# Optimization experiments

Measured on AMD Instinct MI355X. Metric: run time of the kernel, lower is better.

## Reference

```python
import jax, jax.numpy as jnp
import numpy as np

IN_F = 4096
OUT_F = 4096
WBITS = 4      # weight bits
ABITS = 4      # input (activation) bits; T=4 -> L=ceil(15/4)=4 spike levels/step
EPS = 1e-8


def fwht(x):
    """Normalized fast Walsh-Hadamard transform over the last dim (K=1 case of
    matmul_hadU_cuda): y = H_n @ x / sqrt(n), n a power of 2."""
    n = x.shape[-1]
    m = int(np.log2(n))
    shape = x.shape
    x = x.reshape((-1,) + (2,) * m)  # [B, 2,2,...,2]
    for ax in range(1, m + 1):       # fixed log2(n) butterfly stages
        a = jnp.take(x, 0, axis=ax)
        b = jnp.take(x, 1, axis=ax)
        x = jnp.stack([a + b, a - b], axis=ax)
    return x.reshape(shape) * np.float32(1.0 / np.sqrt(n))


def quant_weight(w):
    """Per-output-channel symmetric RTN fake-quant to WBITS, with STE."""
    qmax = 2 ** (WBITS - 1) - 1  # 7
    scale = jnp.maximum(jnp.max(jnp.abs(w), axis=1, keepdims=True) / qmax, EPS)
    q = jnp.clip(jnp.round(w / scale), -qmax - 1, qmax)
    wq = q * scale
    return w + jax.lax.stop_gradient(wq - w)


def quant_act(x):
    """LMHT spiking input quantizer: dynamic asymmetric fake-quant to ABITS.
    Over T steps the neuron emits up to L levels/step, summing to the integer
    code q in [0, 2^ABITS-1]; the (averaged) dequantized output equals
    (q - zp) * scale. STE for gradient."""
    levels = 2 ** ABITS - 1  # 15
    xmin = jnp.min(x)
    xmax = jnp.max(x)
    scale = jnp.maximum((xmax - xmin) / levels, EPS)
    zp = jnp.round(-xmin / scale)
    q = jnp.clip(jnp.round(x / scale) + zp, 0, levels)
    xq = (q - zp) * scale
    return x + jax.lax.stop_gradient(xq - x)


def setup_inputs() -> dict:
    key = jax.random.key(0)
    k1, k2, k3 = jax.random.split(key, 3)
    x = jax.random.normal(k1, (4, 2048, IN_F), dtype=jnp.float32)
    weight = jax.random.normal(k2, (OUT_F, IN_F), dtype=jnp.float32) * 0.02
    bias = jax.random.normal(k3, (OUT_F,), dtype=jnp.float32) * 0.01
    return {"x": x, "weight": weight, "bias": bias}


def reference(x, weight, bias):
    # online full Hadamard rotation of the input
    x = fwht(x)
    # weight fake-quant (W4) and activation fake-quant (A4, LMHT neuron)
    wq = quant_weight(weight)
    xq = quant_act(x)
    # F.linear: out = xq @ wq.T + bias
    out = jnp.einsum('bsi,oi->bso', xq, wq) + bias
    return out
```

## Files before the change

### kernel.cpp

```cpp
#include <hip/hip_runtime.h>
#include <stdint.h>
#include <stddef.h>


typedef __attribute__((ext_vector_type(4))) int int4v;
typedef __attribute__((ext_vector_type(4))) float float4v;

#define EPSQ 1e-8f

__device__ __forceinline__ void fwht_wave(float (&e)[64], int l) {
#pragma unroll
    for (int s = 32; s >= 4; s >>= 1)
#pragma unroll
        for (int j = 0; j < 64; ++j)
            if ((j & s) == 0) {
                float a = e[j], b = e[j + s];
                e[j] = a + b;
                e[j + s] = a - b;
            }
#pragma unroll
    for (int m = 32; m >= 1; m >>= 1) {
        float sgn = (l & m) ? -1.0f : 1.0f;
#pragma unroll
        for (int j = 0; j < 64; ++j) {
            float t = __shfl_xor(e[j], m);
            e[j] = fmaf(sgn, e[j], t);
        }
    }
#pragma unroll
    for (int s = 2; s >= 1; s >>= 1)
#pragma unroll
        for (int j = 0; j < 64; ++j)
            if ((j & s) == 0) {
                float a = e[j], b = e[j + s];
                e[j] = a + b;
                e[j + s] = a - b;
            }
}

__global__ __launch_bounds__(256) void k_fwht_store(
    const float* __restrict__ x, float* __restrict__ y,
    float2* __restrict__ wmm) {
    int l = threadIdx.x & 63, w = threadIdx.x >> 6;
    int row = blockIdx.x * 4 + w;
    const float4v* xv = (const float4v*)(x + (size_t)row * 4096);
    float e[64];
#pragma unroll
    for (int q = 0; q < 16; ++q) {
        float4v v = xv[q * 64 + l];
        e[4 * q + 0] = v[0]; e[4 * q + 1] = v[1];
        e[4 * q + 2] = v[2]; e[4 * q + 3] = v[3];
    }
    fwht_wave(e, l);
#pragma unroll
    for (int j = 0; j < 64; ++j) e[j] *= 0.015625f;

    float4v* yv = (float4v*)(y + (size_t)row * 4096);
#pragma unroll
    for (int q = 0; q < 16; ++q) {
        float4v v;
        v[0] = e[4 * q + 0]; v[1] = e[4 * q + 1];
        v[2] = e[4 * q + 2]; v[3] = e[4 * q + 3];
        yv[q * 64 + l] = v;
    }
    float mn = e[0], mx = e[0];
#pragma unroll
    for (int j = 1; j < 64; ++j) { mn = fminf(mn, e[j]); mx = fmaxf(mx, e[j]); }
#pragma unroll
    for (int m = 32; m >= 1; m >>= 1) {
        mn = fminf(mn, __shfl_xor(mn, m));
        mx = fmaxf(mx, __shfl_xor(mx, m));
    }
    if (l == 0) wmm[row] = make_float2(mn, mx);
}

__global__ __launch_bounds__(256) void k_mmred(const float2* __restrict__ wmm,
                                               float* __restrict__ mm) {
    __shared__ float red[8];
    int t = threadIdx.x;
    float mn = INFINITY, mx = -INFINITY;
    for (int i = t; i < 8192; i += 256) {
        float2 v = wmm[i];
        mn = fminf(mn, v.x);
        mx = fmaxf(mx, v.y);
    }
#pragma unroll
    for (int m = 32; m >= 1; m >>= 1) {
        mn = fminf(mn, __shfl_xor(mn, m));
        mx = fmaxf(mx, __shfl_xor(mx, m));
    }
    if ((t & 63) == 0) { red[(t >> 6) * 2] = mn; red[(t >> 6) * 2 + 1] = mx; }
    __syncthreads();
    if (t == 0) {
#pragma unroll
        for (int wv = 1; wv < 4; ++wv) {
            mn = fminf(mn, red[wv * 2]);
            mx = fmaxf(mx, red[wv * 2 + 1]);
        }
        mm[0] = mn;
        mm[1] = mx;
    }
}

__global__ __launch_bounds__(256) void k_quant_x(
    const float* __restrict__ y, const float* __restrict__ mm,
    int8_t* __restrict__ xq) {
    float xmin = mm[0], xmax = mm[1];
    float scale = fmaxf((xmax - xmin) / 15.0f, EPSQ);
    float zp = rintf(-xmin / scale);
    int izp = (int)zp;

    const float4v* yv = (const float4v*)y;
    int* q = (int*)xq;
    const size_t n4 = (size_t)8192 * 4096 / 4;
    const size_t stride = (size_t)2048 * 256;
    for (size_t i = (size_t)blockIdx.x * 256 + threadIdx.x; i < n4;
         i += stride) {
        float4v v = yv[i];
        int pk = 0;
#pragma unroll
        for (int r = 0; r < 4; ++r) {
            float qq = rintf(v[r] / scale) + zp;
            qq = fminf(fmaxf(qq, 0.0f), 15.0f);
            int code = (int)qq - izp;
            pk |= (code & 0xFF) << (8 * r);
        }
        q[i] = pk;
    }
}

__global__ __launch_bounds__(256) void k_quant_w(
    const float* __restrict__ wgt, int8_t* __restrict__ wq,
    float* __restrict__ sw) {
    __shared__ float red[4];
    int o = blockIdx.x, t = threadIdx.x;
    const float4v* wv = (const float4v*)(wgt + (size_t)o * 4096);
    float4v a0 = wv[t * 4 + 0], a1 = wv[t * 4 + 1],
            a2 = wv[t * 4 + 2], a3 = wv[t * 4 + 3];
    float am = 0.0f;
#pragma unroll
    for (int r = 0; r < 4; ++r)
        am = fmaxf(am, fmaxf(fmaxf(fabsf(a0[r]), fabsf(a1[r])),
                             fmaxf(fabsf(a2[r]), fabsf(a3[r]))));
#pragma unroll
    for (int m = 32; m >= 1; m >>= 1) am = fmaxf(am, __shfl_xor(am, m));
    if ((t & 63) == 0) red[t >> 6] = am;
    __syncthreads();
    am = fmaxf(fmaxf(red[0], red[1]), fmaxf(red[2], red[3]));

    float scale = fmaxf(am / 7.0f, EPSQ);
    if (t == 0) sw[o] = scale;

    int4v pk;
#pragma unroll
    for (int k = 0; k < 4; ++k) {
        float4v a = (k == 0) ? a0 : (k == 1) ? a1 : (k == 2) ? a2 : a3;
        int p = 0;
#pragma unroll
        for (int r = 0; r < 4; ++r) {
            float q = rintf(a[r] / scale);
            q = fminf(fmaxf(q, -8.0f), 7.0f);
            p |= ((int)q & 0xFF) << (8 * r);
        }
        pk[k] = p;
    }
    *(int4v*)(wq + (size_t)o * 4096 + t * 16) = pk;
}

#define BM 128
#define BN 128
#define BKq 64

__global__ __launch_bounds__(256) void k_gemm(
    const int8_t* __restrict__ A,
    const int8_t* __restrict__ B,
    const float* __restrict__ sw, const float* __restrict__ bias,
    const float* __restrict__ mm, float* __restrict__ C) {
    constexpr int N = 4096, K = 4096;
    __shared__ __align__(16) int8_t As[BM * BKq];
    __shared__ __align__(16) int8_t Bs[BN * BKq];

    int tid = threadIdx.x;
    int m0 = (blockIdx.x >> 5) * BM;
    int n0 = (blockIdx.x & 31) * BN;
    int w = tid >> 6, l = tid & 63;
    int wr = w >> 1, wc = w & 1;
    int kg = l >> 4, lr = l & 15;

    int4v acc[4][4] = {};

    for (int k0 = 0; k0 < K; k0 += BKq) {
#pragma unroll
        for (int it = 0; it < 2; ++it) {
            int idx = it * 256 + tid;
            int row = idx >> 2;
            int ccs = (idx & 3) ^ ((row >> 1) & 3);
            __builtin_amdgcn_global_load_lds(
                (const __attribute__((address_space(1))) void*)
                    (A + (size_t)(m0 + row) * K + k0 + ccs * 16),
                (__attribute__((address_space(3))) void*)(As + idx * 16),
                16, 0, 0);
            __builtin_amdgcn_global_load_lds(
                (const __attribute__((address_space(1))) void*)
                    (B + (size_t)(n0 + row) * K + k0 + ccs * 16),
                (__attribute__((address_space(3))) void*)(Bs + idx * 16),
                16, 0, 0);
        }
        __syncthreads();

        int4v af[4], bf[4];
#pragma unroll
        for (int i = 0; i < 4; ++i) {
            int ra = wr * 64 + i * 16 + lr;
            int rb = wc * 64 + i * 16 + lr;
            af[i] = *(const int4v*)(As + ra * BKq +
                                    ((kg ^ ((ra >> 1) & 3)) * 16));
            bf[i] = *(const int4v*)(Bs + rb * BKq +
                                    ((kg ^ ((rb >> 1) & 3)) * 16));
        }
#pragma unroll
        for (int i = 0; i < 4; ++i)
#pragma unroll
            for (int j = 0; j < 4; ++j)
                acc[i][j] = __builtin_amdgcn_mfma_i32_16x16x64_i8(
                    af[i], bf[j], acc[i][j], 0, 0, 0);
        __syncthreads();
    }

    float xmin = mm[0], xmax = mm[1];
    float sx = fmaxf((xmax - xmin) / 15.0f, EPSQ);

#pragma unroll
    for (int j = 0; j < 4; ++j) {
        int col = n0 + wc * 64 + j * 16 + lr;
        float s = sx * sw[col];
        float bz = bias[col];
#pragma unroll
        for (int i = 0; i < 4; ++i) {
            int rowb = m0 + wr * 64 + i * 16 + kg * 4;
#pragma unroll
            for (int r = 0; r < 4; ++r)
                C[(size_t)(rowb + r) * N + col] =
                    (float)acc[i][j][r] * s + bz;
        }
    }
}

extern "C" void kernel_launch(void* const* d_in, const int* in_sizes, int n_in,
                              void* d_out, int out_size, void* d_ws,
                              size_t ws_size, hipStream_t stream) {
    const float* x = (const float*)d_in[0];
    const float* weight = (const float*)d_in[1];
    const float* bias = (const float*)d_in[2];
    float* out = (float*)d_out;

    char* ws = (char*)d_ws;
    float* mm = (float*)ws;
    float2* wmm = (float2*)(ws + 1024);
    float* sw = (float*)(ws + 131072);
    int8_t* xq = (int8_t*)(ws + (1 << 20));
    int8_t* wq = (int8_t*)(ws + (1 << 20) + ((size_t)8192 * 4096));

    float* y = out;

    hipLaunchKernelGGL(k_fwht_store, dim3(2048), dim3(256), 0, stream,
                       x, y, wmm);
    hipLaunchKernelGGL(k_mmred, dim3(1), dim3(256), 0, stream, wmm, mm);
    hipLaunchKernelGGL(k_quant_w, dim3(4096), dim3(256), 0, stream,
                       weight, wq, sw);
    hipLaunchKernelGGL(k_quant_x, dim3(2048), dim3(256), 0, stream,
                       y, mm, xq);
    hipLaunchKernelGGL(k_gemm, dim3(64 * 32), dim3(256), 0, stream,
                       xq, wq, sw, bias, mm, out);
}
```

Measured before the change: 465.9 us.

## Replace cross-lane shuffle FWHT with LDS transpose and two in-register H64 passes

The Walsh-Hadamard transform previously used 6 rounds of 64 cross-lane shuffles per wave. It now does a 64-point butterfly in registers, transposes through a swizzled shared-memory tile, and does a second 64-point butterfly, treating H4096 as H64 ⊗ H64. This removes the shuffle traffic but adds 64 KB of LDS per block, which limits occupancy, and makes the input loads strided scalar reads. The min/max reduction now launches 1024 threads and the activation quantizer uses twice as many blocks.

```diff
diff --git a/kernel.cpp b/kernel.cpp
--- a/kernel.cpp
+++ b/kernel.cpp
@@ -8,9 +8,9 @@
 
 #define EPSQ 1e-8f
 
-__device__ __forceinline__ void fwht_wave(float (&e)[64], int l) {
-#pragma unroll
-    for (int s = 32; s >= 4; s >>= 1)
+__device__ __forceinline__ void h64(float (&e)[64]) {
+#pragma unroll
+    for (int s = 32; s >= 1; s >>= 1)
 #pragma unroll
         for (int j = 0; j < 64; ++j)
             if ((j & s) == 0) {
@@ -18,51 +18,52 @@
                 e[j] = a + b;
                 e[j + s] = a - b;
             }
-#pragma unroll
-    for (int m = 32; m >= 1; m >>= 1) {
-        float sgn = (l & m) ? -1.0f : 1.0f;
-#pragma unroll
-        for (int j = 0; j < 64; ++j) {
-            float t = __shfl_xor(e[j], m);
-            e[j] = fmaf(sgn, e[j], t);
-        }
-    }
-#pragma unroll
-    for (int s = 2; s >= 1; s >>= 1)
-#pragma unroll
-        for (int j = 0; j < 64; ++j)
-            if ((j & s) == 0) {
-                float a = e[j], b = e[j + s];
-                e[j] = a + b;
-                e[j + s] = a - b;
-            }
-}
-
-__global__ __launch_bounds__(256) void k_fwht_store(
+}
+
+__global__ __launch_bounds__(256) void k_fwht(
     const float* __restrict__ x, float* __restrict__ y,
     float2* __restrict__ wmm) {
+    __shared__ float tile[4][4096];
     int l = threadIdx.x & 63, w = threadIdx.x >> 6;
     int row = blockIdx.x * 4 + w;
-    const float4v* xv = (const float4v*)(x + (size_t)row * 4096);
+    const float* xr = x + (size_t)row * 4096;
+
     float e[64];
 #pragma unroll
-    for (int q = 0; q < 16; ++q) {
-        float4v v = xv[q * 64 + l];
-        e[4 * q + 0] = v[0]; e[4 * q + 1] = v[1];
-        e[4 * q + 2] = v[2]; e[4 * q + 3] = v[3];
-    }
-    fwht_wave(e, l);
+    for (int a = 0; a < 64; ++a) e[a] = xr[a * 64 + l];
+
+    h64(e);
+
+    float* T = tile[w];
+#pragma unroll
+    for (int t = 0; t < 16; ++t) {
+        float4v v;
+        v[0] = e[4 * t + 0]; v[1] = e[4 * t + 1];
+        v[2] = e[4 * t + 2]; v[3] = e[4 * t + 3];
+        *(float4v*)(T + l * 64 + 4 * ((t + l) & 15)) = v;
+    }
+    __syncthreads();
+    {
+        int t0 = l >> 2, j0 = l & 3;
+#pragma unroll
+        for (int b = 0; b < 64; ++b)
+            e[b] = T[b * 64 + 4 * ((t0 + b) & 15) + j0];
+    }
+
+    h64(e);
+
 #pragma unroll
     for (int j = 0; j < 64; ++j) e[j] *= 0.015625f;
 
-    float4v* yv = (float4v*)(y + (size_t)row * 4096);
-#pragma unroll
-    for (int q = 0; q < 16; ++q) {
+    float* yr = y + (size_t)row * 4096 + l * 64;
+#pragma unroll
+    for (int t = 0; t < 16; ++t) {
         float4v v;
-        v[0] = e[4 * q + 0]; v[1] = e[4 * q + 1];
-        v[2] = e[4 * q + 2]; v[3] = e[4 * q + 3];
-        yv[q * 64 + l] = v;
-    }
+        v[0] = e[4 * t + 0]; v[1] = e[4 * t + 1];
+        v[2] = e[4 * t + 2]; v[3] = e[4 * t + 3];
+        *(float4v*)(yr + 4 * t) = v;
+    }
+
     float mn = e[0], mx = e[0];
 #pragma unroll
     for (int j = 1; j < 64; ++j) { mn = fminf(mn, e[j]); mx = fmaxf(mx, e[j]); }
@@ -74,12 +75,13 @@
     if (l == 0) wmm[row] = make_float2(mn, mx);
 }
 
-__global__ __launch_bounds__(256) void k_mmred(const float2* __restrict__ wmm,
-                                               float* __restrict__ mm) {
-    __shared__ float red[8];
+__global__ __launch_bounds__(1024) void k_mmred(const float2* __restrict__ wmm,
+                                                float* __restrict__ mm) {
+    __shared__ float red[32];
     int t = threadIdx.x;
     float mn = INFINITY, mx = -INFINITY;
-    for (int i = t; i < 8192; i += 256) {
+#pragma unroll
+    for (int i = t; i < 8192; i += 1024) {
         float2 v = wmm[i];
         mn = fminf(mn, v.x);
         mx = fmaxf(mx, v.y);
@@ -93,7 +95,7 @@
     __syncthreads();
     if (t == 0) {
 #pragma unroll
-        for (int wv = 1; wv < 4; ++wv) {
+        for (int wv = 1; wv < 16; ++wv) {
             mn = fminf(mn, red[wv * 2]);
             mx = fmaxf(mx, red[wv * 2 + 1]);
         }
@@ -113,7 +115,7 @@
     const float4v* yv = (const float4v*)y;
     int* q = (int*)xq;
     const size_t n4 = (size_t)8192 * 4096 / 4;
-    const size_t stride = (size_t)2048 * 256;
+    const size_t stride = (size_t)4096 * 256;
     for (size_t i = (size_t)blockIdx.x * 256 + threadIdx.x; i < n4;
          i += stride) {
         float4v v = yv[i];
@@ -263,12 +265,11 @@
 
     float* y = out;
 
-    hipLaunchKernelGGL(k_fwht_store, dim3(2048), dim3(256), 0, stream,
-                       x, y, wmm);
-    hipLaunchKernelGGL(k_mmred, dim3(1), dim3(256), 0, stream, wmm, mm);
+    hipLaunchKernelGGL(k_fwht, dim3(2048), dim3(256), 0, stream, x, y, wmm);
+    hipLaunchKernelGGL(k_mmred, dim3(1), dim3(1024), 0, stream, wmm, mm);
     hipLaunchKernelGGL(k_quant_w, dim3(4096), dim3(256), 0, stream,
                        weight, wq, sw);
-    hipLaunchKernelGGL(k_quant_x, dim3(2048), dim3(256), 0, stream,
+    hipLaunchKernelGGL(k_quant_x, dim3(4096), dim3(256), 0, stream,
                        y, mm, xq);
     hipLaunchKernelGGL(k_gemm, dim3(64 * 32), dim3(256), 0, stream,
                        xq, wq, sw, bias, mm, out);
```

Result: no change. 473.8 us (+1.7%).
